# Kernel optimization log

Measured on AMD Instinct MI355X. Metric: run time of the kernel, lower is better.

The kernel has to match this reference:

```python
import jax, jax.numpy as jnp
import numpy as np

WIDTH_IN = 8
WIDTH_OUT = 8
STRIDES = (1, 1)
PADDING = 'SAME'


def quantizer(x, width, mode='round', clip=True):
    """Fixed-point quantization to `width` bits in [-1, 1), straight-through estimator.

    mode='round' -> round-to-nearest; mode='floor' -> truncate.
    clip=True saturates to the representable range [-1, 1 - 2^-(width-1)].
    """
    scale = jnp.asarray(2.0 ** (width - 1), x.dtype)
    q = jnp.round(x * scale) if mode == 'round' else jnp.floor(x * scale)
    q = q / scale
    # straight-through: forward uses q, gradient flows as identity
    q = x + jax.lax.stop_gradient(q - x)
    if clip:
        q = jnp.clip(q, -1.0, 1.0 - 1.0 / scale)
    return q


def setup_inputs() -> dict:
    key = jax.random.key(0)
    kx, kw = jax.random.split(key)
    x = jax.random.normal(kx, (32, 112, 112, 64), dtype=jnp.float32)      # NHWC
    kernels = jax.random.normal(kw, (3, 3, 64, 128), dtype=jnp.float32) * 0.05  # HWIO, RandomNormal init
    return {"x": x, "kernels": kernels}


def reference(x, kernels):
    # Method == 'Fixed' path of MyConv2D.call
    xq = quantizer(x, WIDTH_IN, 'round', clip=True)                # quantize activations
    kq = quantizer(kernels, WIDTH_IN, 'round', clip=True)          # quantize weights
    out = jax.lax.conv_general_dilated(
        xq, kq,
        window_strides=STRIDES,
        padding=PADDING,
        dimension_numbers=('NHWC', 'HWIO', 'NHWC'),
    )                                                              # [B, 112, 112, 128]
    out = quantizer(out, WIDTH_OUT, 'floor', clip=False)           # quantize output, truncating
    return out
```

## Files before the change

kernel.cpp:

```cpp
#include <hip/hip_runtime.h>

#define NIMG 32
#define H 112
#define W 112
#define CI 64
#define CO 128

typedef __attribute__((ext_vector_type(8))) __bf16 bf16x8;
typedef __attribute__((ext_vector_type(4))) float f32x4;
typedef __attribute__((ext_vector_type(4))) short short4v;
typedef __attribute__((ext_vector_type(4))) int int4v;
typedef __attribute__((ext_vector_type(2))) int int2v;

__device__ __forceinline__ short q8bits(float v) {
    float t = rintf(v * 128.0f);
    t = fminf(fmaxf(t, -128.0f), 127.0f);
    union { float f; unsigned u; } cv; cv.f = t;
    return (short)(cv.u >> 16);
}
__device__ __forceinline__ int q8i(float v) {
    float t = rintf(v * 128.0f);
    t = fminf(fmaxf(t, -128.0f), 127.0f);
    return (int)t;
}

__global__ __launch_bounds__(256) void quant_pack_w_i8(const float* __restrict__ w,
                                                       signed char* __restrict__ bp) {
    int idx = blockIdx.x * 256 + threadIdx.x;
    int j  = idx & 15;
    int l  = (idx >> 4) & 63;
    int nt = (idx >> 10) & 7;
    int kk = idx >> 13;
    int k = kk * 64 + (l >> 4) * 16 + j;
    int n = nt * 16 + (l & 15);
    bp[idx] = (signed char)q8i(w[k * CO + n]);
}

__global__ __launch_bounds__(256) void quant_x_i8(const float* __restrict__ x,
                                                  signed char* __restrict__ xq) {
    size_t i = ((size_t)blockIdx.x * 256 + threadIdx.x) * 8;
    float4 v0 = *(const float4*)&x[i];
    float4 v1 = *(const float4*)&x[i + 4];
    int b0 = (q8i(v0.x) & 255) | ((q8i(v0.y) & 255) << 8) |
             ((q8i(v0.z) & 255) << 16) | (q8i(v0.w) << 24);
    int b1 = (q8i(v1.x) & 255) | ((q8i(v1.y) & 255) << 8) |
             ((q8i(v1.z) & 255) << 16) | (q8i(v1.w) << 24);
    int2v p; p.x = b0; p.y = b1;
    *(int2v*)&xq[i] = p;
}

#define RB 7296

__global__ __launch_bounds__(256, 3) void conv_i8(const signed char* __restrict__ xq,
                                                  const signed char* __restrict__ bp,
                                                  float* __restrict__ out) {
    __shared__ __align__(16) signed char xs[3 * RB];
    int bid0 = blockIdx.x;
    int bid = (bid0 & 7) * 448 + (bid0 >> 3);
    int n = bid / H;
    int h = bid - n * H;
    int tid  = threadIdx.x;
    int lane = tid & 63;
    int wave = tid >> 6;

    const signed char* base = xq + (size_t)(n * H) * (W * CI);
    for (int idx = wave; idx < 21; idx += 4) {
        int row = idx / 7;
        int i = idx - row * 7;
        int hr = h - 1 + row;
        if ((unsigned)hr < (unsigned)H) {
            const signed char* g = base + (size_t)hr * (W * CI) + i * 1024 + lane * 16;
            __builtin_amdgcn_global_load_lds(
                (const __attribute__((address_space(1))) void*)g,
                (__attribute__((address_space(3))) void*)(xs + row * RB + 64 + i * 1024),
                16, 0, 0);
        }
    }

    int nt0 = wave * 2;
    const int4v* bp4 = (const int4v*)bp;
    int4v breg[9][2];
    #pragma unroll
    for (int kk = 0; kk < 9; ++kk) {
        breg[kk][0] = bp4[(kk * 8 + nt0    ) * 64 + lane];
        breg[kk][1] = bp4[(kk * 8 + nt0 + 1) * 64 + lane];
    }

    if (h == 0)
        for (int t = tid; t < 456; t += 256) *(int4v*)&xs[t * 16] = (int4v){0, 0, 0, 0};
    if (h == H - 1)
        for (int t = tid; t < 456; t += 256) *(int4v*)&xs[2 * RB + t * 16] = (int4v){0, 0, 0, 0};
    if (tid < 24) {
        int r2 = tid >> 3, ci = tid & 7;
        int c = (ci & 4) ? 113 : 0;
        *(int4v*)&xs[r2 * RB + c * 64 + (ci & 3) * 16] = (int4v){0, 0, 0, 0};
    }
    __syncthreads();

    int lane15 = lane & 15;
    int hi     = lane >> 4;

    int4v acc[7][2];
    #pragma unroll
    for (int mt = 0; mt < 7; ++mt) {
        acc[mt][0] = (int4v){0, 0, 0, 0};
        acc[mt][1] = (int4v){0, 0, 0, 0};
    }

    #pragma unroll
    for (int r = 0; r < 3; ++r) {
        #pragma unroll
        for (int s = 0; s < 3; ++s) {
            int kk = r * 3 + s;
            int abase = r * RB + (s + lane15) * 64 + hi * 16;
            #pragma unroll
            for (int mt = 0; mt < 7; ++mt) {
                int4v a = *(const int4v*)&xs[abase + mt * 1024];
                acc[mt][0] = __builtin_amdgcn_mfma_i32_16x16x64_i8(a, breg[kk][0], acc[mt][0], 0, 0, 0);
                acc[mt][1] = __builtin_amdgcn_mfma_i32_16x16x64_i8(a, breg[kk][1], acc[mt][1], 0, 0, 0);
            }
        }
    }

    float* orow = out + (size_t)((n * H + h) * W) * CO;
    int co0  = wave * 32 + lane15;
    int rowb = hi * 4;
    #pragma unroll
    for (int mt = 0; mt < 7; ++mt)
        #pragma unroll
        for (int t = 0; t < 2; ++t)
            #pragma unroll
            for (int rg = 0; rg < 4; ++rg) {
                int m = mt * 16 + rowb + rg;
                orow[m * CO + co0 + t * 16] =
                    (float)(acc[mt][t][rg] >> 7) * 0.0078125f;
            }
}

__global__ __launch_bounds__(256) void quant_pack_w(const float* __restrict__ w,
                                                    short* __restrict__ bp) {
    int idx = blockIdx.x * 256 + threadIdx.x;
    int j    = idx & 7;
    int lane = (idx >> 3) & 63;
    int nt   = (idx >> 9) & 7;
    int kt   = idx >> 12;
    int k = kt * 32 + (lane >> 4) * 8 + j;
    int n = nt * 16 + (lane & 15);
    bp[idx] = q8bits(w[k * CO + n]);
}

#define LDSW 114
#define LDST 72
__global__ __launch_bounds__(256, 3) void conv_fb(const float* __restrict__ x,
                                                  const short* __restrict__ bp,
                                                  float* __restrict__ out) {
    __shared__ short xs[3 * LDSW * LDST];
    int bid = blockIdx.x;
    int n = bid / H;
    int h = bid - n * H;
    int tid = threadIdx.x;
    const float* xin = x + (size_t)n * (H * W * CI);
    for (int r = 0; r < 3; ++r) {
        int hrow = h + r - 1;
        bool rowok = ((unsigned)hrow < (unsigned)H);
        const float* srow = xin + (size_t)hrow * (W * CI);
        for (int t = tid; t < LDSW * 16; t += 256) {
            int c = t >> 4;
            int ci4 = (t & 15) << 2;
            int wcol = c - 1;
            float4 v = {0.f, 0.f, 0.f, 0.f};
            if (rowok && (unsigned)wcol < (unsigned)W)
                v = *(const float4*)&srow[wcol * CI + ci4];
            short4v sv;
            sv.x = q8bits(v.x); sv.y = q8bits(v.y);
            sv.z = q8bits(v.z); sv.w = q8bits(v.w);
            *(short4v*)&xs[(r * LDSW + c) * LDST + ci4] = sv;
        }
    }
    __syncthreads();
    int lane = tid & 63;
    int wave = tid >> 6;
    int laneoff = (lane & 15) * LDST + (lane >> 4) * 8;
    const bf16x8* bfr = (const bf16x8*)bp;
    int nt0 = wave * 2;
    f32x4 acc[7][2];
    #pragma unroll
    for (int mt = 0; mt < 7; ++mt) {
        acc[mt][0] = (f32x4){0.f, 0.f, 0.f, 0.f};
        acc[mt][1] = (f32x4){0.f, 0.f, 0.f, 0.f};
    }
    #pragma unroll
    for (int kk = 0; kk < 18; ++kk) {
        int rs = kk >> 1;
        int r = rs / 3;
        int s = rs - r * 3;
        bf16x8 b0 = bfr[(kk * 8 + nt0    ) * 64 + lane];
        bf16x8 b1 = bfr[(kk * 8 + nt0 + 1) * 64 + lane];
        int abase = (r * LDSW + s) * LDST + (kk & 1) * 32 + laneoff;
        #pragma unroll
        for (int mt = 0; mt < 7; ++mt) {
            bf16x8 a = *(const bf16x8*)&xs[abase + mt * 16 * LDST];
            acc[mt][0] = __builtin_amdgcn_mfma_f32_16x16x32_bf16(a, b0, acc[mt][0], 0, 0, 0);
            acc[mt][1] = __builtin_amdgcn_mfma_f32_16x16x32_bf16(a, b1, acc[mt][1], 0, 0, 0);
        }
    }
    float* orow = out + (size_t)(n * H + h) * (W * CO);
    int colc = wave * 32 + (lane & 15);
    int rowb = (lane >> 4) * 4;
    #pragma unroll
    for (int mt = 0; mt < 7; ++mt)
        #pragma unroll
        for (int t2 = 0; t2 < 2; ++t2)
            #pragma unroll
            for (int rg = 0; rg < 4; ++rg) {
                int m = mt * 16 + rowb + rg;
                orow[m * CO + colc + t2 * 16] =
                    floorf(acc[mt][t2][rg] * 0.0078125f) * 0.0078125f;
            }
}

extern "C" void kernel_launch(void* const* d_in, const int* in_sizes, int n_in,
                              void* d_out, int out_size, void* d_ws, size_t ws_size,
                              hipStream_t stream) {
    const float* x = (const float*)d_in[0];
    const float* w = (const float*)d_in[1];
    float* out = (float*)d_out;

    const size_t BPI8_BYTES = 73728;
    const size_t XQ8_BYTES  = (size_t)NIMG * H * W * CI;

    if (ws_size >= BPI8_BYTES + XQ8_BYTES) {
        signed char* bp8 = (signed char*)d_ws;
        signed char* xq8 = (signed char*)d_ws + BPI8_BYTES;
        quant_pack_w_i8<<<288, 256, 0, stream>>>(w, bp8);
        quant_x_i8<<<12544, 256, 0, stream>>>(x, xq8);
        conv_i8<<<NIMG * H, 256, 0, stream>>>(xq8, bp8, out);
    } else {
        short* bp = (short*)d_ws;
        quant_pack_w<<<288, 256, 0, stream>>>(w, bp);
        conv_fb<<<NIMG * H, 256, 0, stream>>>(x, bp, out);
    }
}
```

Measured before the change: 306.4 us.

## Fuse activation quantization into int8 conv with 4-row ring-buffered LDS tiles

Removes the separate activation quantization kernel and its int8 intermediate buffer. The conv kernel now reads float input directly, quantizes it into LDS, and processes 4 output rows per block using a 4-slot ring of input rows. The next row is prefetched and quantized while the MFMA loop for the current row runs. LDS writes use an XOR swizzle to reduce bank conflicts. This trades fewer kernel launches and less global traffic, since each input row is read about 1.5 times instead of 3, for more LDS per block, extra registers for the prefetch, and fewer blocks in the grid.

```diff
diff --git a/kernel.cpp b/kernel.cpp
--- a/kernel.cpp
+++ b/kernel.cpp
@@ -5,12 +5,13 @@
 #define W 112
 #define CI 64
 #define CO 128
+#define ROWS 4
+#define GPI 28
 
 typedef __attribute__((ext_vector_type(8))) __bf16 bf16x8;
 typedef __attribute__((ext_vector_type(4))) float f32x4;
 typedef __attribute__((ext_vector_type(4))) short short4v;
 typedef __attribute__((ext_vector_type(4))) int int4v;
-typedef __attribute__((ext_vector_type(2))) int int2v;
 
 __device__ __forceinline__ short q8bits(float v) {
     float t = rintf(v * 128.0f);
@@ -36,46 +37,22 @@
     bp[idx] = (signed char)q8i(w[k * CO + n]);
 }
 
-__global__ __launch_bounds__(256) void quant_x_i8(const float* __restrict__ x,
-                                                  signed char* __restrict__ xq) {
-    size_t i = ((size_t)blockIdx.x * 256 + threadIdx.x) * 8;
-    float4 v0 = *(const float4*)&x[i];
-    float4 v1 = *(const float4*)&x[i + 4];
-    int b0 = (q8i(v0.x) & 255) | ((q8i(v0.y) & 255) << 8) |
-             ((q8i(v0.z) & 255) << 16) | (q8i(v0.w) << 24);
-    int b1 = (q8i(v1.x) & 255) | ((q8i(v1.y) & 255) << 8) |
-             ((q8i(v1.z) & 255) << 16) | (q8i(v1.w) << 24);
-    int2v p; p.x = b0; p.y = b1;
-    *(int2v*)&xq[i] = p;
-}
-
 #define RB 7296
 
-__global__ __launch_bounds__(256, 3) void conv_i8(const signed char* __restrict__ xq,
-                                                  const signed char* __restrict__ bp,
-                                                  float* __restrict__ out) {
-    __shared__ __align__(16) signed char xs[3 * RB];
+__global__ __launch_bounds__(256, 3) void conv_fused(const float* __restrict__ x,
+                                                     const signed char* __restrict__ bp,
+                                                     float* __restrict__ out) {
+    __shared__ __align__(16) signed char xs[4 * RB];
     int bid0 = blockIdx.x;
-    int bid = (bid0 & 7) * 448 + (bid0 >> 3);
-    int n = bid / H;
-    int h = bid - n * H;
+    int bid = (bid0 & 7) * 112 + (bid0 >> 3);
+    int n  = bid / GPI;
+    int rg = bid - n * GPI;
+    int h0 = rg * ROWS;
     int tid  = threadIdx.x;
     int lane = tid & 63;
     int wave = tid >> 6;
-
-    const signed char* base = xq + (size_t)(n * H) * (W * CI);
-    for (int idx = wave; idx < 21; idx += 4) {
-        int row = idx / 7;
-        int i = idx - row * 7;
-        int hr = h - 1 + row;
-        if ((unsigned)hr < (unsigned)H) {
-            const signed char* g = base + (size_t)hr * (W * CI) + i * 1024 + lane * 16;
-            __builtin_amdgcn_global_load_lds(
-                (const __attribute__((address_space(1))) void*)g,
-                (__attribute__((address_space(3))) void*)(xs + row * RB + 64 + i * 1024),
-                16, 0, 0);
-        }
-    }
+    int lane15 = lane & 15;
+    int hi     = lane >> 4;
 
     int nt0 = wave * 2;
     const int4v* bp4 = (const int4v*)bp;
@@ -86,55 +63,109 @@
         breg[kk][1] = bp4[(kk * 8 + nt0 + 1) * 64 + lane];
     }
 
-    if (h == 0)
-        for (int t = tid; t < 456; t += 256) *(int4v*)&xs[t * 16] = (int4v){0, 0, 0, 0};
-    if (h == H - 1)
-        for (int t = tid; t < 456; t += 256) *(int4v*)&xs[2 * RB + t * 16] = (int4v){0, 0, 0, 0};
-    if (tid < 24) {
-        int r2 = tid >> 3, ci = tid & 7;
-        int c = (ci & 4) ? 113 : 0;
-        *(int4v*)&xs[r2 * RB + c * 64 + (ci & 3) * 16] = (int4v){0, 0, 0, 0};
+    if (tid < 32)
+        *(int4v*)&xs[(tid >> 3) * RB + ((tid & 4) ? 113 : 0) * 64 + (tid & 3) * 16] =
+            (int4v){0, 0, 0, 0};
+
+    #pragma unroll
+    for (int r = 0; r < 3; ++r) {
+        int hr = h0 - 1 + r;
+        signed char* dst = &xs[((hr + 1) & 3) * RB];
+        if ((unsigned)hr < (unsigned)H) {
+            const float* src = x + ((size_t)(n * H + hr) * W) * CI;
+            float4 v[7];
+            #pragma unroll
+            for (int k = 0; k < 7; ++k) v[k] = *(const float4*)&src[k * 1024 + tid * 4];
+            #pragma unroll
+            for (int k = 0; k < 7; ++k) {
+                int b = (q8i(v[k].x) & 255) | ((q8i(v[k].y) & 255) << 8) |
+                        ((q8i(v[k].z) & 255) << 16) | (q8i(v[k].w) << 24);
+                int L = k * 1024 + tid * 4;
+                int col = 1 + (L >> 6);
+                int ci  = L & 63;
+                *(int*)&dst[col * 64 + (((ci >> 4) ^ (col & 3)) << 4) + (ci & 15)] = b;
+            }
+        } else {
+            #pragma unroll
+            for (int k = 0; k < 7; ++k) {
+                int L = k * 1024 + tid * 4;
+                int col = 1 + (L >> 6);
+                int ci  = L & 63;
+                *(int*)&dst[col * 64 + (((ci >> 4) ^ (col & 3)) << 4) + (ci & 15)] = 0;
+            }
+        }
     }
     __syncthreads();
 
-    int lane15 = lane & 15;
-    int hi     = lane >> 4;
-
-    int4v acc[7][2];
-    #pragma unroll
-    for (int mt = 0; mt < 7; ++mt) {
-        acc[mt][0] = (int4v){0, 0, 0, 0};
-        acc[mt][1] = (int4v){0, 0, 0, 0};
-    }
-
-    #pragma unroll
-    for (int r = 0; r < 3; ++r) {
-        #pragma unroll
-        for (int s = 0; s < 3; ++s) {
-            int kk = r * 3 + s;
-            int abase = r * RB + (s + lane15) * 64 + hi * 16;
-            #pragma unroll
-            for (int mt = 0; mt < 7; ++mt) {
-                int4v a = *(const int4v*)&xs[abase + mt * 1024];
-                acc[mt][0] = __builtin_amdgcn_mfma_i32_16x16x64_i8(a, breg[kk][0], acc[mt][0], 0, 0, 0);
-                acc[mt][1] = __builtin_amdgcn_mfma_i32_16x16x64_i8(a, breg[kk][1], acc[mt][1], 0, 0, 0);
-            }
-        }
-    }
-
-    float* orow = out + (size_t)((n * H + h) * W) * CO;
-    int co0  = wave * 32 + lane15;
-    int rowb = hi * 4;
-    #pragma unroll
-    for (int mt = 0; mt < 7; ++mt)
-        #pragma unroll
-        for (int t = 0; t < 2; ++t)
-            #pragma unroll
-            for (int rg = 0; rg < 4; ++rg) {
-                int m = mt * 16 + rowb + rg;
-                orow[m * CO + co0 + t * 16] =
-                    (float)(acc[mt][t][rg] >> 7) * 0.0078125f;
-            }
+    for (int t = 0; t < ROWS; ++t) {
+        float4 pv[7];
+        int hpre = h0 + t + 2;
+        bool do_pre = (t < ROWS - 1);
+        bool pre_valid = do_pre && (hpre < H);
+        const float* psrc = x + ((size_t)(n * H + hpre) * W) * CI;
+        if (pre_valid) {
+            #pragma unroll
+            for (int k = 0; k < 5; ++k) pv[k] = *(const float4*)&psrc[k * 1024 + tid * 4];
+        }
+
+        int4v acc[7][2];
+        #pragma unroll
+        for (int mt = 0; mt < 7; ++mt) {
+            acc[mt][0] = (int4v){0, 0, 0, 0};
+            acc[mt][1] = (int4v){0, 0, 0, 0};
+        }
+        #pragma unroll
+        for (int r = 0; r < 3; ++r) {
+            int sbase = ((t + r) & 3) * RB;
+            #pragma unroll
+            for (int s = 0; s < 3; ++s) {
+                int kk = r * 3 + s;
+                int col = s + lane15;
+                int abase = sbase + col * 64 + ((hi ^ (col & 3)) << 4);
+                #pragma unroll
+                for (int mt = 0; mt < 7; ++mt) {
+                    int4v a = *(const int4v*)&xs[abase + mt * 1024];
+                    acc[mt][0] = __builtin_amdgcn_mfma_i32_16x16x64_i8(a, breg[kk][0], acc[mt][0], 0, 0, 0);
+                    acc[mt][1] = __builtin_amdgcn_mfma_i32_16x16x64_i8(a, breg[kk][1], acc[mt][1], 0, 0, 0);
+                }
+            }
+        }
+
+        if (pre_valid) {
+            #pragma unroll
+            for (int k = 5; k < 7; ++k) pv[k] = *(const float4*)&psrc[k * 1024 + tid * 4];
+        }
+        if (do_pre) {
+            signed char* dst = &xs[((t + 3) & 3) * RB];
+            #pragma unroll
+            for (int k = 0; k < 7; ++k) {
+                int b = 0;
+                if (pre_valid)
+                    b = (q8i(pv[k].x) & 255) | ((q8i(pv[k].y) & 255) << 8) |
+                        ((q8i(pv[k].z) & 255) << 16) | (q8i(pv[k].w) << 24);
+                int L = k * 1024 + tid * 4;
+                int col = 1 + (L >> 6);
+                int ci  = L & 63;
+                *(int*)&dst[col * 64 + (((ci >> 4) ^ (col & 3)) << 4) + (ci & 15)] = b;
+            }
+        }
+
+        float* orow = out + (size_t)((n * H + h0 + t) * W) * CO;
+        int co0  = wave * 32 + lane15;
+        int rowb = hi * 4;
+        #pragma unroll
+        for (int mt = 0; mt < 7; ++mt)
+            #pragma unroll
+            for (int tt = 0; tt < 2; ++tt)
+                #pragma unroll
+                for (int rgi = 0; rgi < 4; ++rgi) {
+                    int m = mt * 16 + rowb + rgi;
+                    orow[m * CO + co0 + tt * 16] =
+                        (float)(acc[mt][tt][rgi] >> 7) * 0.0078125f;
+                }
+
+        if (t < ROWS - 1) __syncthreads();
+    }
 }
 
 __global__ __launch_bounds__(256) void quant_pack_w(const float* __restrict__ w,
@@ -212,10 +243,10 @@
         #pragma unroll
         for (int t2 = 0; t2 < 2; ++t2)
             #pragma unroll
-            for (int rg = 0; rg < 4; ++rg) {
-                int m = mt * 16 + rowb + rg;
+            for (int rgi = 0; rgi < 4; ++rgi) {
+                int m = mt * 16 + rowb + rgi;
                 orow[m * CO + colc + t2 * 16] =
-                    floorf(acc[mt][t2][rg] * 0.0078125f) * 0.0078125f;
+                    floorf(acc[mt][t2][rgi] * 0.0078125f) * 0.0078125f;
             }
 }
 
@@ -227,14 +258,11 @@
     float* out = (float*)d_out;
 
     const size_t BPI8_BYTES = 73728;
-    const size_t XQ8_BYTES  = (size_t)NIMG * H * W * CI;
-
-    if (ws_size >= BPI8_BYTES + XQ8_BYTES) {
+
+    if (ws_size >= BPI8_BYTES) {
         signed char* bp8 = (signed char*)d_ws;
-        signed char* xq8 = (signed char*)d_ws + BPI8_BYTES;
         quant_pack_w_i8<<<288, 256, 0, stream>>>(w, bp8);
-        quant_x_i8<<<12544, 256, 0, stream>>>(x, xq8);
-        conv_i8<<<NIMG * H, 256, 0, stream>>>(xq8, bp8, out);
+        conv_fused<<<NIMG * GPI, 256, 0, stream>>>(x, bp8, out);
     } else {
         short* bp = (short*)d_ws;
         quant_pack_w<<<288, 256, 0, stream>>>(w, bp);
```

Result: slower. 437.3 us (+42.7%).
